# Kernel tuning notes

Hardware: AMD Instinct MI355X
Metric: run time of the kernel (lower is better)

## Reference

```python
import jax, jax.numpy as jnp
import numpy as np

B, T, D = 512, 128, 768
CD, SD, P = 192, 128, 128
FEAT = CD + SD + 1  # 321
LN_EPS = 1e-5


def setup_inputs() -> dict:
    key = jax.random.key(0)
    ks = jax.random.split(key, 10)
    return {
        'H': jax.random.normal(ks[0], (B, T, D), jnp.float32),
        'tt': jax.random.randint(ks[1], (B, T), 0, 2, jnp.int64),
        'attn': jnp.ones((B, T), jnp.int64),
        'Wc': jax.random.normal(ks[2], (CD, 2 * D), jnp.float32) * 0.02,
        'bc': jax.random.normal(ks[3], (CD,), jnp.float32) * 0.02,
        'Ws': jax.random.normal(ks[4], (SD, 2 * D), jnp.float32) * 0.02,
        'bs': jax.random.normal(ks[5], (SD,), jnp.float32) * 0.02,
        'gate': jnp.array([0.5], jnp.float32),
        'ln_g': jnp.ones((FEAT,), jnp.float32),
        'ln_b': jnp.zeros((FEAT,), jnp.float32),
        'Wcls': jax.random.normal(ks[6], (2, FEAT), jnp.float32) * 0.02,
        'bcls': jax.random.normal(ks[7], (2,), jnp.float32) * 0.02,
        'dirs': jax.random.normal(ks[8], (P, D), jnp.float32),
    }


def reference(H, tt, attn, Wc, bc, Ws, bs, gate, ln_g, ln_b, Wcls, bcls, dirs):
    dt = H.dtype
    cls = H[:, 0]                                   # [B, D]
    mask0 = (tt == 0) & (attn == 1)                 # [B, T]
    mask1 = (tt == 1) & (attn == 1)

    def mmean(mask):
        mf = mask.astype(dt)
        s = jnp.einsum('btd,bt->bd', H, mf)
        cnt = jnp.maximum(mask.sum(1, keepdims=True), 1).astype(dt)
        return s / cnt

    rep = jnp.concatenate([cls, mmean(mask0) - mmean(mask1)], axis=1)  # [B, 2D]
    C = rep @ Wc.T + bc
    S = rep @ Ws.T + bs
    g = jax.nn.sigmoid(gate)                        # [1]
    fused = jnp.concatenate([C * (1 - g), S * g], axis=1)  # [B, CD+SD]

    # batched max-sliced W1: project, push masked tokens to +inf, sort along T
    dirs_n = dirs / jnp.linalg.norm(dirs, axis=1, keepdims=True)
    proj = jnp.einsum('btd,pd->btp', H, dirs_n)     # [B, T, P]
    inf = jnp.asarray(jnp.inf, dt)
    xp = jnp.sort(jnp.where(mask0[:, :, None], proj, inf), axis=1)
    yp = jnp.sort(jnp.where(mask1[:, :, None], proj, inf), axis=1)
    n0 = mask0.sum(1)
    n1 = mask1.sum(1)
    mm = jnp.minimum(n0, n1)                        # [B] ragged truncation length
    valid = (jnp.arange(T)[None, :] < mm[:, None])[:, :, None]  # [B, T, 1]
    xs = jnp.where(valid, xp, 0.0)
    ys = jnp.where(valid, yp, 0.0)
    diff = jnp.abs(xs - ys).sum(1) / jnp.maximum(mm, 1)[:, None].astype(dt)  # [B, P]
    d_ot = diff.max(1, keepdims=True)               # [B, 1]

    feat = jnp.concatenate([fused, d_ot], axis=1)   # [B, 321]
    mu = feat.mean(-1, keepdims=True)
    var = feat.var(-1, keepdims=True)
    normed = (feat - mu) / jnp.sqrt(var + LN_EPS) * ln_g + ln_b
    logits = normed @ Wcls.T + bcls                 # [B, 2]

    ortho = jnp.mean((Wc @ Ws.T) ** 2)
    return logits, ortho
```

## Files before the change

### kernel.cpp

```cpp
#include <hip/hip_runtime.h>
#include <hip/hip_bf16.h>

constexpr int B_ = 512;
constexpr int T_ = 128;
constexpr int D_ = 768;
constexpr int CD_ = 192;
constexpr int SD_ = 128;
constexpr int P_ = 128;
constexpr int FEAT_ = 321;
constexpr float LN_EPS_ = 1e-5f;

constexpr size_t REP_SZ   = (size_t)B_ * 2 * D_;
constexpr size_t DN16_FLT = (size_t)P_ * D_ / 2;

typedef __attribute__((ext_vector_type(8))) short short8;
typedef __attribute__((ext_vector_type(4))) float f32x4;

__device__ __forceinline__ unsigned short f2bf(float x) {
    unsigned u = __float_as_uint(x);
    return (unsigned short)((u + 0x7FFFu + ((u >> 16) & 1u)) >> 16);
}
__device__ __forceinline__ float bf2f(unsigned short h) {
    return __uint_as_float((unsigned)h << 16);
}

__global__ __launch_bounds__(256) void k_dirs(const float* __restrict__ dirs,
                                              unsigned short* __restrict__ dn16) {
    int p = blockIdx.x;
    int tid = threadIdx.x;
    float s = 0.f;
    for (int d = tid; d < D_; d += 256) {
        float v = dirs[(size_t)p * D_ + d];
        s = fmaf(v, v, s);
    }
    __shared__ float red[256];
    red[tid] = s;
    __syncthreads();
    for (int off = 128; off > 0; off >>= 1) {
        if (tid < off) red[tid] += red[tid + off];
        __syncthreads();
    }
    float inv = 1.0f / sqrtf(red[0]);
    for (int d = tid; d < D_; d += 256) {
        dn16[(size_t)p * D_ + d] = f2bf(dirs[(size_t)p * D_ + d] * inv);
    }
}

constexpr int NIT_ = 24;
constexpr int BUF_U16_ = 8192;
constexpr int HT_STR_ = 136;

__global__ __launch_bounds__(512, 2) void k_projsort(const float* __restrict__ H,
                                                     const int* __restrict__ tt,
                                                     const int* __restrict__ attn,
                                                     const unsigned short* __restrict__ dn16,
                                                     float* __restrict__ rep,
                                                     float* __restrict__ d_ot) {
    const int b = blockIdx.x;
    const int tid = threadIdx.x;

    __shared__ __align__(16) unsigned short stage[2 * BUF_U16_];
    __shared__ __align__(16) unsigned short Ht[32 * HT_STR_];
    __shared__ __align__(16) unsigned short proj16[T_ * 128];
    __shared__ __align__(16) unsigned short mask16[2 * T_];
    __shared__ float m0s[T_], m1s[T_];
    __shared__ unsigned char pos_s[T_];
    __shared__ int ncnt[2];
    __shared__ float dred[512];

    unsigned char* xb = (unsigned char*)stage;
    unsigned char* yb = xb + 64 * 128;

    const float* Hb = H + (size_t)b * T_ * D_;
    const int srow = tid >> 2;
    const int scp  = tid & 3;
    const int sclog = scp ^ ((srow >> 1) & 3);
    const float* gA = Hb + (size_t)srow * D_ + sclog * 8;
    const unsigned short* gB = dn16 + (size_t)srow * D_ + sclog * 8;
    const int dOff = srow * 32 + scp * 8;

    float4 a0A = *reinterpret_cast<const float4*>(gA);
    float4 a1A = *reinterpret_cast<const float4*>(gA + 4);
    short8 bvA = *reinterpret_cast<const short8*>(gB);
    float4 a0B = *reinterpret_cast<const float4*>(gA + 32);
    float4 a1B = *reinterpret_cast<const float4*>(gA + 36);
    short8 bvB = *reinterpret_cast<const short8*>(gB + 32);

    if (tid < 2) ncnt[tid] = 0;
    __syncthreads();
    if (tid < T_) {
        int t = tt[b * T_ + tid];
        int a = attn[b * T_ + tid];
        float m0 = (t == 0 && a == 1) ? 1.f : 0.f;
        float m1 = (t == 1 && a == 1) ? 1.f : 0.f;
        m0s[tid] = m0;
        m1s[tid] = m1;
        mask16[tid] = (m0 > 0.f) ? 0x3F80u : 0u;
        mask16[T_ + tid] = (m1 > 0.f) ? 0x3F80u : 0u;
        if (m0 > 0.f) atomicAdd(&ncnt[0], 1);
        if (m1 > 0.f) atomicAdd(&ncnt[1], 1);
    }
    __syncthreads();
    const int n0 = ncnt[0], n1 = ncnt[1];
    const int ntot = n0 + n1;
    const float inv0 = 1.f / (float)max(n0, 1);
    const float inv1 = 1.f / (float)max(n1, 1);
    if (tid < T_) {
        float me0 = m0s[tid], me1 = m1s[tid];
        unsigned char pp = 0xFF;
        if (me0 > 0.f || me1 > 0.f) {
            bool g1 = (me1 > 0.f);
            const float* ms = g1 ? m1s : m0s;
            int pos = g1 ? n0 : 0;
            for (int j = 0; j < tid; ++j) pos += (ms[j] > 0.f) ? 1 : 0;
            pp = (unsigned char)pos;
        }
        pos_s[tid] = pp;
    }
    __syncthreads();

    const int wv = tid >> 6;
    const int wr = wv >> 2;
    const int wc = wv & 3;
    const int lane = tid & 63;
    const int fr = lane & 15;
    const int kg = lane >> 4;
    const int fk = kg * 8;
    const int ck = (kg ^ ((fr >> 1) & 3)) * 8;
    const int baseA = (64 * wr + fr) * 32 + ck;
    const int baseB = 4096 + (32 * wc + 16 * 0 + fr) * 32 + ck;
    const bool repw = (wv >= 6);
    const int jf = wv & 1;
    float* repb = rep + (size_t)b * 2 * D_;

    f32x4 acc[4][2];
#pragma unroll
    for (int m = 0; m < 4; ++m)
#pragma unroll
        for (int n = 0; n < 2; ++n) acc[m][n] = (f32x4){0.f, 0.f, 0.f, 0.f};

    auto body = [&](int it, unsigned short* sb, float4& pa0, float4& pa1, short8& pbv) {
        short8 w;
        w[0] = (short)f2bf(pa0.x); w[1] = (short)f2bf(pa0.y);
        w[2] = (short)f2bf(pa0.z); w[3] = (short)f2bf(pa0.w);
        w[4] = (short)f2bf(pa1.x); w[5] = (short)f2bf(pa1.y);
        w[6] = (short)f2bf(pa1.z); w[7] = (short)f2bf(pa1.w);
        *reinterpret_cast<short8*>(sb + dOff) = w;
        *reinterpret_cast<short8*>(sb + 4096 + dOff) = pbv;
#pragma unroll
        for (int j = 0; j < 8; ++j)
            Ht[(sclog * 8 + j) * HT_STR_ + srow] = (unsigned short)w[j];
        if (srow == 0) {
            *reinterpret_cast<float4*>(repb + it * 32 + sclog * 8) = pa0;
            *reinterpret_cast<float4*>(repb + it * 32 + sclog * 8 + 4) = pa1;
        }
        if (it + 2 < NIT_) {
            pa0 = *reinterpret_cast<const float4*>(gA + (it + 2) * 32);
            pa1 = *reinterpret_cast<const float4*>(gA + (it + 2) * 32 + 4);
            pbv = *reinterpret_cast<const short8*>(gB + (it + 2) * 32);
        }
        asm volatile("s_waitcnt lgkmcnt(0)" ::: "memory");
        __builtin_amdgcn_s_barrier();
        asm volatile("" ::: "memory");

        short8 af[4], bf_[2];
#pragma unroll
        for (int m = 0; m < 4; ++m)
            af[m] = *reinterpret_cast<const short8*>(sb + baseA + 512 * m);
#pragma unroll
        for (int n = 0; n < 2; ++n)
            bf_[n] = *reinterpret_cast<const short8*>(sb + baseB + 512 * n);
#pragma unroll
        for (int m = 0; m < 4; ++m)
#pragma unroll
            for (int n = 0; n < 2; ++n)
                acc[m][n] = __builtin_amdgcn_mfma_f32_16x16x32_bf16(af[m], bf_[n], acc[m][n], 0, 0, 0);

        if (repw) {
            f32x4 ar = (f32x4){0.f, 0.f, 0.f, 0.f};
#pragma unroll
            for (int tc = 0; tc < 4; ++tc) {
                short8 am = {0, 0, 0, 0, 0, 0, 0, 0};
                if (fr < 2) am = *reinterpret_cast<const short8*>(&mask16[fr * T_ + tc * 32 + fk]);
                short8 bm = *reinterpret_cast<const short8*>(&Ht[(16 * jf + fr) * HT_STR_ + tc * 32 + fk]);
                ar = __builtin_amdgcn_mfma_f32_16x16x32_bf16(am, bm, ar, 0, 0, 0);
            }
            if (lane < 16) repb[D_ + it * 32 + jf * 16 + lane] = ar[0] * inv0 - ar[1] * inv1;
        }
        asm volatile("" ::: "memory");
        __builtin_amdgcn_s_barrier();
        asm volatile("" ::: "memory");
    };

    for (int i2 = 0; i2 < NIT_ / 2; ++i2) {
        body(2 * i2,     stage,            a0A, a1A, bvA);
        body(2 * i2 + 1, stage + BUF_U16_, a0B, a1B, bvB);
    }

#pragma unroll
    for (int m = 0; m < 4; ++m) {
        int row0 = 64 * wr + 16 * m + kg * 4;
#pragma unroll
        for (int r = 0; r < 4; ++r) {
            int pp = pos_s[row0 + r];
            if (pp != 0xFF) {
#pragma unroll
                for (int n = 0; n < 2; ++n) {
                    int col = 32 * wc + 16 * n + fr;
                    unsigned bb = f2bf(acc[m][n][r]);
                    unsigned su = bb ^ ((bb >> 15) ? 0xFFFFu : 0x8000u);
                    proj16[pp * 128 + col] = (unsigned short)su;
                }
            }
        }
    }
    __syncthreads();

    const int mmv = min(n0, n1);
    const int c = tid & 127;
    const int q = tid >> 7;
#pragma unroll
    for (int pass = 0; pass < 2; ++pass) {
        const int pbase = q * 32 + pass * 16;
        unsigned kv[16];
        int cnt[16];
#pragma unroll
        for (int ii = 0; ii < 16; ++ii) {
            int p = pbase + ii;
            unsigned key = 0xFFFFFFFFu;
            if (p < ntot) {
                unsigned su = proj16[p * 128 + c];
                key = ((unsigned)(p >= n0) << 31) | (su << 8) | (unsigned)p;
            }
            kv[ii] = key;
            cnt[ii] = 0;
        }
        int lo, hi;
        if (pbase + 16 <= n0) { lo = 0;  hi = n0;   }
        else if (pbase >= n0) { lo = n0; hi = ntot; }
        else                  { lo = 0;  hi = ntot; }
        for (int j = lo; j < hi; ++j) {
            unsigned su = proj16[j * 128 + c];
            unsigned kw = ((unsigned)(j >= n0) << 31) | (su << 8) | (unsigned)j;
#pragma unroll
            for (int ii = 0; ii < 16; ++ii) cnt[ii] += (kw < kv[ii]) ? 1 : 0;
        }
#pragma unroll
        for (int ii = 0; ii < 16; ++ii) {
            int p = pbase + ii;
            if (p < ntot) {
                int rank = cnt[ii] - ((p >= n0 && lo == 0) ? n0 : 0);
                if (rank < mmv) {
                    unsigned char* buf = (p >= n0) ? yb : xb;
                    buf[rank * 128 + c] = (unsigned char)p;
                }
            }
        }
    }
    __syncthreads();

    float part = 0.f;
    for (int r = q; r < mmv; r += 4) {
        unsigned sx = proj16[(int)xb[r * 128 + c] * 128 + c];
        unsigned sy = proj16[(int)yb[r * 128 + c] * 128 + c];
        unsigned bx = sx ^ ((sx >> 15) ? 0x8000u : 0xFFFFu);
        unsigned by = sy ^ ((sy >> 15) ? 0x8000u : 0xFFFFu);
        part += fabsf(bf2f((unsigned short)bx) - bf2f((unsigned short)by));
    }
    dred[tid] = part;
    __syncthreads();
    if (tid < 128) {
        float invm = 1.f / (float)max(mmv, 1);
        dred[tid] = (dred[tid] + dred[tid + 128] + dred[tid + 256] + dred[tid + 384]) * invm;
    }
    __syncthreads();
    if (tid < 64) {
        float m = fmaxf(dred[tid], dred[tid + 64]);
#pragma unroll
        for (int off = 32; off > 0; off >>= 1) m = fmaxf(m, __shfl_xor(m, off));
        if (tid == 0) d_ot[b] = m;
    }
}

__global__ __launch_bounds__(320) void k_head(const float* __restrict__ rep,
                                              const float* __restrict__ Wc,
                                              const float* __restrict__ bc,
                                              const float* __restrict__ Ws,
                                              const float* __restrict__ bs,
                                              const float* __restrict__ gate,
                                              const float* __restrict__ lng,
                                              const float* __restrict__ lnb,
                                              const float* __restrict__ Wcls,
                                              const float* __restrict__ bcls,
                                              const float* __restrict__ d_ot,
                                              float* __restrict__ out) {
    int b0 = blockIdx.x * 4;
    int tid = threadIdx.x;
    __shared__ __align__(16) float repS[4 * 1536];
    __shared__ float featS[4 * FEAT_];

    const float4* repg = reinterpret_cast<const float4*>(rep + (size_t)b0 * 1536);
    float4* repl = reinterpret_cast<float4*>(repS);
    for (int i = tid; i < 1536; i += 320) repl[i] = repg[i];
    __syncthreads();

    float g = 1.f / (1.f + expf(-gate[0]));

    {
        int o = tid;
        bool isC = o < CD_;
        const float* w = isC ? (Wc + (size_t)o * 1536) : (Ws + (size_t)(o - CD_) * 1536);
        float bias = isC ? bc[o] : bs[o - CD_];
        float scale = isC ? (1.f - g) : g;
        const float4* w4 = reinterpret_cast<const float4*>(w);
        float a0 = 0.f, a1 = 0.f, a2 = 0.f, a3 = 0.f;
        for (int k4 = 0; k4 < 384; ++k4) {
            float4 wv = w4[k4];
            float4 r0 = repl[k4];
            float4 r1 = repl[384 + k4];
            float4 r2 = repl[768 + k4];
            float4 r3 = repl[1152 + k4];
            a0 += fmaf(wv.x, r0.x, fmaf(wv.y, r0.y, fmaf(wv.z, r0.z, wv.w * r0.w)));
            a1 += fmaf(wv.x, r1.x, fmaf(wv.y, r1.y, fmaf(wv.z, r1.z, wv.w * r1.w)));
            a2 += fmaf(wv.x, r2.x, fmaf(wv.y, r2.y, fmaf(wv.z, r2.z, wv.w * r2.w)));
            a3 += fmaf(wv.x, r3.x, fmaf(wv.y, r3.y, fmaf(wv.z, r3.z, wv.w * r3.w)));
        }
        featS[0 * FEAT_ + o] = (a0 + bias) * scale;
        featS[1 * FEAT_ + o] = (a1 + bias) * scale;
        featS[2 * FEAT_ + o] = (a2 + bias) * scale;
        featS[3 * FEAT_ + o] = (a3 + bias) * scale;
    }
    if (tid < 4) featS[tid * FEAT_ + 320] = d_ot[b0 + tid];
    __syncthreads();

    int w = tid >> 6, lane = tid & 63;
    if (w < 4) {
        const float* f = featS + w * FEAT_;
        float s = 0.f, s2 = 0.f;
        for (int i = lane; i < FEAT_; i += 64) {
            float v = f[i];
            s += v;
            s2 = fmaf(v, v, s2);
        }
#pragma unroll
        for (int off = 32; off > 0; off >>= 1) {
            s += __shfl_xor(s, off);
            s2 += __shfl_xor(s2, off);
        }
        float mu = s * (1.f / (float)FEAT_);
        float var = fmaxf(s2 * (1.f / (float)FEAT_) - mu * mu, 0.f);
        float rstd = 1.0f / sqrtf(var + LN_EPS_);
        float l0 = 0.f, l1 = 0.f;
        for (int i = lane; i < FEAT_; i += 64) {
            float nv = (f[i] - mu) * rstd * lng[i] + lnb[i];
            l0 = fmaf(nv, Wcls[i], l0);
            l1 = fmaf(nv, Wcls[FEAT_ + i], l1);
        }
#pragma unroll
        for (int off = 32; off > 0; off >>= 1) {
            l0 += __shfl_xor(l0, off);
            l1 += __shfl_xor(l1, off);
        }
        if (lane == 0) {
            out[(size_t)(b0 + w) * 2 + 0] = l0 + bcls[0];
            out[(size_t)(b0 + w) * 2 + 1] = l1 + bcls[1];
        }
    }
}

__global__ __launch_bounds__(256) void k_ortho(const float* __restrict__ Wc,
                                               const float* __restrict__ Ws,
                                               float* __restrict__ part) {
    int i = blockIdx.x;
    int tid = threadIdx.x;
    __shared__ float wrow[1536];
    __shared__ float tmp[256];
    for (int k = tid; k < 1536; k += 256) wrow[k] = Wc[(size_t)i * 1536 + k];
    __syncthreads();
    int j = tid & 127, h = tid >> 7;
    const float* wsr = Ws + (size_t)j * 1536 + h * 768;
    const float* wr = wrow + h * 768;
    float s = 0.f;
    for (int k = 0; k < 768; ++k) s = fmaf(wr[k], wsr[k], s);
    tmp[tid] = s;
    __syncthreads();
    if (tid < 128) {
        float d = tmp[tid] + tmp[tid + 128];
        tmp[tid] = d * d;
    }
    __syncthreads();
    for (int off = 64; off > 0; off >>= 1) {
        if (tid < off) tmp[tid] += tmp[tid + off];
        __syncthreads();
    }
    if (tid == 0) part[i] = tmp[0];
}

__global__ __launch_bounds__(256) void k_ortho2(const float* __restrict__ part,
                                                float* __restrict__ out) {
    int tid = threadIdx.x;
    __shared__ float red[256];
    red[tid] = (tid < CD_) ? part[tid] : 0.f;
    __syncthreads();
    for (int off = 128; off > 0; off >>= 1) {
        if (tid < off) red[tid] += red[tid + off];
        __syncthreads();
    }
    if (tid == 0) out[(size_t)B_ * 2] = red[0] / (float)(CD_ * SD_);
}

extern "C" void kernel_launch(void* const* d_in, const int* in_sizes, int n_in,
                              void* d_out, int out_size, void* d_ws, size_t ws_size,
                              hipStream_t stream) {
    const float* H    = (const float*)d_in[0];
    const int*   tt   = (const int*)d_in[1];
    const int*   attn = (const int*)d_in[2];
    const float* Wc   = (const float*)d_in[3];
    const float* bc   = (const float*)d_in[4];
    const float* Ws   = (const float*)d_in[5];
    const float* bs   = (const float*)d_in[6];
    const float* gate = (const float*)d_in[7];
    const float* lng  = (const float*)d_in[8];
    const float* lnb  = (const float*)d_in[9];
    const float* Wcls = (const float*)d_in[10];
    const float* bcls = (const float*)d_in[11];
    const float* dirs = (const float*)d_in[12];

    float* ws    = (float*)d_ws;
    float* rep   = ws;
    unsigned short* dn16 = (unsigned short*)(ws + REP_SZ);
    float* dot   = ws + REP_SZ + DN16_FLT;
    float* part  = dot + B_;
    float* out   = (float*)d_out;

    k_dirs<<<P_, 256, 0, stream>>>(dirs, dn16);
    k_projsort<<<B_, 512, 0, stream>>>(H, tt, attn, dn16, rep, dot);
    k_head<<<B_ / 4, 320, 0, stream>>>(rep, Wc, bc, Ws, bs, gate, lng, lnb, Wcls, bcls, dot, out);
    k_ortho<<<CD_, 256, 0, stream>>>(Wc, Ws, part);
    k_ortho2<<<1, 256, 0, stream>>>(part, out);
}
```

Before: 191.3 us.

## Split projection-sort across two blocks per batch over direction halves

The fused projection and sort kernel now launches two 256-thread blocks per batch row, each handling 64 of the 128 projection directions. Partial max distances go to a two-entry buffer that the head kernel reduces. Mask counts and positions now come from wavefront ballots and popcounts instead of a serial prefix loop. The separate transposed H buffer is dropped, with the masked-mean MMA reading the staged tile directly through strided gathers. The aim is more blocks, higher occupancy and less LDS per block, at the cost of each block reloading the full H tile for its batch row.

```diff
diff --git a/kernel.cpp b/kernel.cpp
--- a/kernel.cpp
+++ b/kernel.cpp
@@ -47,90 +47,97 @@
 }
 
 constexpr int NIT_ = 24;
-constexpr int BUF_U16_ = 8192;
-constexpr int HT_STR_ = 136;
-
-__global__ __launch_bounds__(512, 2) void k_projsort(const float* __restrict__ H,
+constexpr int BUFU_ = 6144;
+
+__global__ __launch_bounds__(256, 4) void k_projsort(const float* __restrict__ H,
                                                      const int* __restrict__ tt,
                                                      const int* __restrict__ attn,
                                                      const unsigned short* __restrict__ dn16,
                                                      float* __restrict__ rep,
-                                                     float* __restrict__ d_ot) {
+                                                     float* __restrict__ dot2) {
     const int b = blockIdx.x;
+    const int y = blockIdx.y;
+    const int p0 = y * 64;
     const int tid = threadIdx.x;
-
-    __shared__ __align__(16) unsigned short stage[2 * BUF_U16_];
-    __shared__ __align__(16) unsigned short Ht[32 * HT_STR_];
-    __shared__ __align__(16) unsigned short proj16[T_ * 128];
-    __shared__ __align__(16) unsigned short mask16[2 * T_];
-    __shared__ float m0s[T_], m1s[T_];
-    __shared__ unsigned char pos_s[T_];
-    __shared__ int ncnt[2];
-    __shared__ float dred[512];
-
+    const int lane = tid & 63;
+    const int w = tid >> 6;
+
+    __shared__ __align__(16) unsigned short stage[2 * BUFU_];
+    __shared__ __align__(16) unsigned short proj16[8192];
     unsigned char* xb = (unsigned char*)stage;
-    unsigned char* yb = xb + 64 * 128;
-
-    const float* Hb = H + (size_t)b * T_ * D_;
-    const int srow = tid >> 2;
-    const int scp  = tid & 3;
-    const int sclog = scp ^ ((srow >> 1) & 3);
-    const float* gA = Hb + (size_t)srow * D_ + sclog * 8;
-    const unsigned short* gB = dn16 + (size_t)srow * D_ + sclog * 8;
-    const int dOff = srow * 32 + scp * 8;
-
-    float4 a0A = *reinterpret_cast<const float4*>(gA);
-    float4 a1A = *reinterpret_cast<const float4*>(gA + 4);
-    short8 bvA = *reinterpret_cast<const short8*>(gB);
-    float4 a0B = *reinterpret_cast<const float4*>(gA + 32);
-    float4 a1B = *reinterpret_cast<const float4*>(gA + 36);
-    short8 bvB = *reinterpret_cast<const short8*>(gB + 32);
-
-    if (tid < 2) ncnt[tid] = 0;
-    __syncthreads();
-    if (tid < T_) {
-        int t = tt[b * T_ + tid];
-        int a = attn[b * T_ + tid];
-        float m0 = (t == 0 && a == 1) ? 1.f : 0.f;
-        float m1 = (t == 1 && a == 1) ? 1.f : 0.f;
-        m0s[tid] = m0;
-        m1s[tid] = m1;
-        mask16[tid] = (m0 > 0.f) ? 0x3F80u : 0u;
-        mask16[T_ + tid] = (m1 > 0.f) ? 0x3F80u : 0u;
-        if (m0 > 0.f) atomicAdd(&ncnt[0], 1);
-        if (m1 > 0.f) atomicAdd(&ncnt[1], 1);
-    }
-    __syncthreads();
-    const int n0 = ncnt[0], n1 = ncnt[1];
+    unsigned char* yb = xb + 4096;
+    float* dred = (float*)&stage[4096];
+
+    const int srow = tid >> 1;
+    const int cpair = (tid & 1) * 2;
+    const int swz = (srow >> 1) & 3;
+    const int lo_log = (cpair ^ swz) & 2;
+    const float* gA = H + (size_t)b * T_ * D_ + (size_t)srow * D_ + lo_log * 8;
+    const int brow = tid & 63;
+    const int bphys = tid >> 6;
+    const int bl = bphys ^ ((brow >> 1) & 3);
+    const unsigned short* gB = dn16 + (size_t)(p0 + brow) * D_ + bl * 8;
+    const int aOff = srow * 32;
+    const int physA0 = lo_log ^ swz;
+
+    float4 fa0 = *reinterpret_cast<const float4*>(gA);
+    float4 fa1 = *reinterpret_cast<const float4*>(gA + 4);
+    float4 fa2 = *reinterpret_cast<const float4*>(gA + 8);
+    float4 fa3 = *reinterpret_cast<const float4*>(gA + 12);
+    short8 bv = *reinterpret_cast<const short8*>(gB);
+
+    const int wr = w & 1;
+    const int wc2 = w >> 1;
+    const int myt = 64 * wr + lane;
+    int v_tt = tt[b * T_ + myt];
+    int v_at = attn[b * T_ + myt];
+    bool m0 = (v_tt == 0) && (v_at == 1);
+    bool m1 = (v_tt == 1) && (v_at == 1);
+    unsigned long long bal0 = __ballot(m0);
+    unsigned long long bal1 = __ballot(m1);
+    if (w < 2 && lane == 0) {
+        ((unsigned long long*)stage)[w * 2] = bal0;
+        ((unsigned long long*)stage)[w * 2 + 1] = bal1;
+    }
+    if (tid < 128) {
+        proj16[tid] = m0 ? 0x3F80u : 0u;
+        proj16[128 + tid] = m1 ? 0x3F80u : 0u;
+    }
+    __syncthreads();
+    const unsigned long long lo0 = ((unsigned long long*)stage)[0];
+    const unsigned long long lo1 = ((unsigned long long*)stage)[1];
+    const unsigned long long hi0 = ((unsigned long long*)stage)[2];
+    const unsigned long long hi1 = ((unsigned long long*)stage)[3];
+    const int n0 = __popcll(lo0) + __popcll(hi0);
+    const int n1 = __popcll(lo1) + __popcll(hi1);
     const int ntot = n0 + n1;
     const float inv0 = 1.f / (float)max(n0, 1);
     const float inv1 = 1.f / (float)max(n1, 1);
-    if (tid < T_) {
-        float me0 = m0s[tid], me1 = m1s[tid];
-        unsigned char pp = 0xFF;
-        if (me0 > 0.f || me1 > 0.f) {
-            bool g1 = (me1 > 0.f);
-            const float* ms = g1 ? m1s : m0s;
-            int pos = g1 ? n0 : 0;
-            for (int j = 0; j < tid; ++j) pos += (ms[j] > 0.f) ? 1 : 0;
-            pp = (unsigned char)pos;
-        }
-        pos_s[tid] = pp;
-    }
-    __syncthreads();
-
-    const int wv = tid >> 6;
-    const int wr = wv >> 2;
-    const int wc = wv & 3;
-    const int lane = tid & 63;
+    unsigned long long below = (lane == 63) ? 0xFFFFFFFFFFFFFFFFull >> 1
+                                            : ((1ull << lane) - 1ull);
+    below = (1ull << lane) - 1ull;
+    int mypos = 0xFF;
+    if (m0) mypos = (wr ? __popcll(lo0) : 0) + __popcll((wr ? hi0 : lo0) & below);
+    else if (m1) mypos = n0 + (wr ? __popcll(lo1) : 0) + __popcll((wr ? hi1 : lo1) & below);
+    __syncthreads();
+
     const int fr = lane & 15;
     const int kg = lane >> 4;
-    const int fk = kg * 8;
-    const int ck = (kg ^ ((fr >> 1) & 3)) * 8;
-    const int baseA = (64 * wr + fr) * 32 + ck;
-    const int baseB = 4096 + (32 * wc + 16 * 0 + fr) * 32 + ck;
-    const bool repw = (wv >= 6);
-    const int jf = wv & 1;
+    int addrA[4], addrB[2];
+#pragma unroll
+    for (int m = 0; m < 4; ++m) {
+        int row = 64 * wr + 16 * m + fr;
+        addrA[m] = row * 32 + (kg ^ ((row >> 1) & 3)) * 8;
+    }
+#pragma unroll
+    for (int n = 0; n < 2; ++n) {
+        int row = 32 * wc2 + 16 * n + fr;
+        addrB[n] = 4096 + row * 32 + (kg ^ ((row >> 1) & 3)) * 8;
+    }
+    const bool repy = (y == 0);
+    const int grp = w & 1;
+    const int dl = grp * 16 + fr;
+    const int dch = dl >> 3, dsub = dl & 7;
     float* repb = rep + (size_t)b * 2 * D_;
 
     f32x4 acc[4][2];
@@ -139,25 +146,34 @@
 #pragma unroll
         for (int n = 0; n < 2; ++n) acc[m][n] = (f32x4){0.f, 0.f, 0.f, 0.f};
 
-    auto body = [&](int it, unsigned short* sb, float4& pa0, float4& pa1, short8& pbv) {
-        short8 w;
-        w[0] = (short)f2bf(pa0.x); w[1] = (short)f2bf(pa0.y);
-        w[2] = (short)f2bf(pa0.z); w[3] = (short)f2bf(pa0.w);
-        w[4] = (short)f2bf(pa1.x); w[5] = (short)f2bf(pa1.y);
-        w[6] = (short)f2bf(pa1.z); w[7] = (short)f2bf(pa1.w);
-        *reinterpret_cast<short8*>(sb + dOff) = w;
-        *reinterpret_cast<short8*>(sb + 4096 + dOff) = pbv;
-#pragma unroll
-        for (int j = 0; j < 8; ++j)
-            Ht[(sclog * 8 + j) * HT_STR_ + srow] = (unsigned short)w[j];
-        if (srow == 0) {
-            *reinterpret_cast<float4*>(repb + it * 32 + sclog * 8) = pa0;
-            *reinterpret_cast<float4*>(repb + it * 32 + sclog * 8 + 4) = pa1;
-        }
-        if (it + 2 < NIT_) {
-            pa0 = *reinterpret_cast<const float4*>(gA + (it + 2) * 32);
-            pa1 = *reinterpret_cast<const float4*>(gA + (it + 2) * 32 + 4);
-            pbv = *reinterpret_cast<const short8*>(gB + (it + 2) * 32);
+    for (int it = 0; it < NIT_; ++it) {
+        const int base = (it & 1) * BUFU_;
+        short8 w0, w1;
+        w0[0] = (short)f2bf(fa0.x); w0[1] = (short)f2bf(fa0.y);
+        w0[2] = (short)f2bf(fa0.z); w0[3] = (short)f2bf(fa0.w);
+        w0[4] = (short)f2bf(fa1.x); w0[5] = (short)f2bf(fa1.y);
+        w0[6] = (short)f2bf(fa1.z); w0[7] = (short)f2bf(fa1.w);
+        w1[0] = (short)f2bf(fa2.x); w1[1] = (short)f2bf(fa2.y);
+        w1[2] = (short)f2bf(fa2.z); w1[3] = (short)f2bf(fa2.w);
+        w1[4] = (short)f2bf(fa3.x); w1[5] = (short)f2bf(fa3.y);
+        w1[6] = (short)f2bf(fa3.z); w1[7] = (short)f2bf(fa3.w);
+        *reinterpret_cast<short8*>(&stage[base + aOff + physA0 * 8]) = w0;
+        *reinterpret_cast<short8*>(&stage[base + aOff + (physA0 ^ 1) * 8]) = w1;
+        *reinterpret_cast<short8*>(&stage[base + 4096 + brow * 32 + bphys * 8]) = bv;
+        if (repy && srow == 0) {
+            float* cd = repb + it * 32 + lo_log * 8;
+            *reinterpret_cast<float4*>(cd)     = fa0;
+            *reinterpret_cast<float4*>(cd + 4) = fa1;
+            *reinterpret_cast<float4*>(cd + 8) = fa2;
+            *reinterpret_cast<float4*>(cd + 12) = fa3;
+        }
+        if (it + 1 < NIT_) {
+            int k = (it + 1) * 32;
+            fa0 = *reinterpret_cast<const float4*>(gA + k);
+            fa1 = *reinterpret_cast<const float4*>(gA + k + 4);
+            fa2 = *reinterpret_cast<const float4*>(gA + k + 8);
+            fa3 = *reinterpret_cast<const float4*>(gA + k + 12);
+            bv = *reinterpret_cast<const short8*>(gB + k);
         }
         asm volatile("s_waitcnt lgkmcnt(0)" ::: "memory");
         __builtin_amdgcn_s_barrier();
@@ -166,50 +182,52 @@
         short8 af[4], bf_[2];
 #pragma unroll
         for (int m = 0; m < 4; ++m)
-            af[m] = *reinterpret_cast<const short8*>(sb + baseA + 512 * m);
+            af[m] = *reinterpret_cast<const short8*>(&stage[base + addrA[m]]);
 #pragma unroll
         for (int n = 0; n < 2; ++n)
-            bf_[n] = *reinterpret_cast<const short8*>(sb + baseB + 512 * n);
+            bf_[n] = *reinterpret_cast<const short8*>(&stage[base + addrB[n]]);
 #pragma unroll
         for (int m = 0; m < 4; ++m)
 #pragma unroll
             for (int n = 0; n < 2; ++n)
                 acc[m][n] = __builtin_amdgcn_mfma_f32_16x16x32_bf16(af[m], bf_[n], acc[m][n], 0, 0, 0);
 
-        if (repw) {
+        if (repy && (((it & 1) == 0) == (w < 2))) {
             f32x4 ar = (f32x4){0.f, 0.f, 0.f, 0.f};
 #pragma unroll
             for (int tc = 0; tc < 4; ++tc) {
+                int tbase = tc * 32 + kg * 8;
                 short8 am = {0, 0, 0, 0, 0, 0, 0, 0};
-                if (fr < 2) am = *reinterpret_cast<const short8*>(&mask16[fr * T_ + tc * 32 + fk]);
-                short8 bm = *reinterpret_cast<const short8*>(&Ht[(16 * jf + fr) * HT_STR_ + tc * 32 + fk]);
+                if (fr < 2) am = *reinterpret_cast<const short8*>(&proj16[fr * 128 + tbase]);
+                short8 bm;
+#pragma unroll
+                for (int j = 0; j < 8; ++j) {
+                    int t = tbase + j;
+                    bm[j] = (short)stage[base + t * 32 + (dch ^ ((t >> 1) & 3)) * 8 + dsub];
+                }
                 ar = __builtin_amdgcn_mfma_f32_16x16x32_bf16(am, bm, ar, 0, 0, 0);
             }
-            if (lane < 16) repb[D_ + it * 32 + jf * 16 + lane] = ar[0] * inv0 - ar[1] * inv1;
+            if (lane < 16)
+                repb[D_ + it * 32 + grp * 16 + lane] = ar[0] * inv0 - ar[1] * inv1;
         }
         asm volatile("" ::: "memory");
         __builtin_amdgcn_s_barrier();
         asm volatile("" ::: "memory");
-    };
-
-    for (int i2 = 0; i2 < NIT_ / 2; ++i2) {
-        body(2 * i2,     stage,            a0A, a1A, bvA);
-        body(2 * i2 + 1, stage + BUF_U16_, a0B, a1B, bvB);
     }
 
 #pragma unroll
     for (int m = 0; m < 4; ++m) {
-        int row0 = 64 * wr + 16 * m + kg * 4;
 #pragma unroll
         for (int r = 0; r < 4; ++r) {
-            int pp = pos_s[row0 + r];
+            int rowlane = 16 * m + kg * 4 + r;
+            int pp = __shfl(mypos, rowlane);
             if (pp != 0xFF) {
 #pragma unroll
                 for (int n = 0; n < 2; ++n) {
-                    int col = 32 * wc + 16 * n + fr;
+                    int col = 32 * wc2 + 16 * n + fr;
                     unsigned bb = f2bf(acc[m][n][r]);
                     unsigned su = bb ^ ((bb >> 15) ? 0xFFFFu : 0x8000u);
-                    proj16[pp * 128 + col] = (unsigned short)su;
+                    proj16[pp * 64 + col] = (unsigned short)su;
                 }
             }
         }
@@ -217,8 +235,8 @@
     __syncthreads();
 
     const int mmv = min(n0, n1);
-    const int c = tid & 127;
-    const int q = tid >> 7;
+    const int c = tid & 63;
+    const int q = tid >> 6;
 #pragma unroll
     for (int pass = 0; pass < 2; ++pass) {
         const int pbase = q * 32 + pass * 16;
@@ -229,7 +247,7 @@
             int p = pbase + ii;
             unsigned key = 0xFFFFFFFFu;
             if (p < ntot) {
-                unsigned su = proj16[p * 128 + c];
+                unsigned su = proj16[p * 64 + c];
                 key = ((unsigned)(p >= n0) << 31) | (su << 8) | (unsigned)p;
             }
             kv[ii] = key;
@@ -240,7 +258,7 @@
         else if (pbase >= n0) { lo = n0; hi = ntot; }
         else                  { lo = 0;  hi = ntot; }
         for (int j = lo; j < hi; ++j) {
-            unsigned su = proj16[j * 128 + c];
+            unsigned su = proj16[j * 64 + c];
             unsigned kw = ((unsigned)(j >= n0) << 31) | (su << 8) | (unsigned)j;
 #pragma unroll
             for (int ii = 0; ii < 16; ++ii) cnt[ii] += (kw < kv[ii]) ? 1 : 0;
@@ -252,7 +270,7 @@
                 int rank = cnt[ii] - ((p >= n0 && lo == 0) ? n0 : 0);
                 if (rank < mmv) {
                     unsigned char* buf = (p >= n0) ? yb : xb;
-                    buf[rank * 128 + c] = (unsigned char)p;
+                    buf[rank * 64 + c] = (unsigned char)p;
                 }
             }
         }
@@ -261,24 +279,21 @@
 
     float part = 0.f;
     for (int r = q; r < mmv; r += 4) {
-        unsigned sx = proj16[(int)xb[r * 128 + c] * 128 + c];
-        unsigned sy = proj16[(int)yb[r * 128 + c] * 128 + c];
+        unsigned sx = proj16[(int)xb[r * 64 + c] * 64 + c];
+        unsigned sy = proj16[(int)yb[r * 64 + c] * 64 + c];
         unsigned bx = sx ^ ((sx >> 15) ? 0x8000u : 0xFFFFu);
-        unsigned by = sy ^ ((sy >> 15) ? 0x8000u : 0xFFFFu);
-        part += fabsf(bf2f((unsigned short)bx) - bf2f((unsigned short)by));
+        unsigned byv = sy ^ ((sy >> 15) ? 0x8000u : 0xFFFFu);
+        part += fabsf(bf2f((unsigned short)bx) - bf2f((unsigned short)byv));
     }
     dred[tid] = part;
     __syncthreads();
-    if (tid < 128) {
+    if (tid < 64) {
         float invm = 1.f / (float)max(mmv, 1);
-        dred[tid] = (dred[tid] + dred[tid + 128] + dred[tid + 256] + dred[tid + 384]) * invm;
-    }
-    __syncthreads();
-    if (tid < 64) {
-        float m = fmaxf(dred[tid], dred[tid + 64]);
+        float s = (dred[tid] + dred[tid + 64] + dred[tid + 128] + dred[tid + 192]) * invm;
+        float m = s;
 #pragma unroll
         for (int off = 32; off > 0; off >>= 1) m = fmaxf(m, __shfl_xor(m, off));
-        if (tid == 0) d_ot[b] = m;
+        if (tid == 0) dot2[b * 2 + y] = m;
     }
 }
 
@@ -292,7 +307,7 @@
                                               const float* __restrict__ lnb,
                                               const float* __restrict__ Wcls,
                                               const float* __restrict__ bcls,
-                                              const float* __restrict__ d_ot,
+                                              const float* __restrict__ dot2,
                                               float* __restrict__ out) {
     int b0 = blockIdx.x * 4;
     int tid = threadIdx.x;
@@ -330,7 +345,10 @@
         featS[2 * FEAT_ + o] = (a2 + bias) * scale;
         featS[3 * FEAT_ + o] = (a3 + bias) * scale;
     }
-    if (tid < 4) featS[tid * FEAT_ + 320] = d_ot[b0 + tid];
+    if (tid < 4) {
+        int bb = b0 + tid;
+        featS[tid * FEAT_ + 320] = fmaxf(dot2[bb * 2], dot2[bb * 2 + 1]);
+    }
     __syncthreads();
 
     int w = tid >> 6, lane = tid & 63;
@@ -429,13 +447,13 @@
     float* ws    = (float*)d_ws;
     float* rep   = ws;
     unsigned short* dn16 = (unsigned short*)(ws + REP_SZ);
-    float* dot   = ws + REP_SZ + DN16_FLT;
-    float* part  = dot + B_;
+    float* dot2  = ws + REP_SZ + DN16_FLT;
+    float* part  = dot2 + 2 * B_;
     float* out   = (float*)d_out;
 
     k_dirs<<<P_, 256, 0, stream>>>(dirs, dn16);
-    k_projsort<<<B_, 512, 0, stream>>>(H, tt, attn, dn16, rep, dot);
-    k_head<<<B_ / 4, 320, 0, stream>>>(rep, Wc, bc, Ws, bs, gate, lng, lnb, Wcls, bcls, dot, out);
+    k_projsort<<<dim3(B_, 2), 256, 0, stream>>>(H, tt, attn, dn16, rep, dot2);
+    k_head<<<B_ / 4, 320, 0, stream>>>(rep, Wc, bc, Ws, bs, gate, lng, lnb, Wcls, bcls, dot2, out);
     k_ortho<<<CD_, 256, 0, stream>>>(Wc, Ws, part);
     k_ortho2<<<1, 256, 0, stream>>>(part, out);
 }
```

After: 208.2 us. +8.8%, slower.

## Split projection into bf16 prep kernel and direct-to-LDS async MFMA pipeline

Applied to the files above, without the earlier changes.

Adds a k_prep kernel that streams H once, writes the CLS and masked-mean rep rows, and stores a pre-swizzled bf16 copy of H in workspace. k_projsort then reads bf16 H and dirs with global_load_lds into a triple-buffered LDS ring, and computes token positions with wave ballots instead of a serial prefix loop. The goal is to take the fp32-to-bf16 conversion, the transposed Ht staging and the mask MFMA out of the inner loop and to overlap loads with compute. In exchange it adds an extra write and read of a bf16 H copy through global memory, and may need to run in batch chunks sized by the workspace.

```diff
diff --git a/kernel.cpp b/kernel.cpp
--- a/kernel.cpp
+++ b/kernel.cpp
@@ -12,6 +12,8 @@
 
 constexpr size_t REP_SZ   = (size_t)B_ * 2 * D_;
 constexpr size_t DN16_FLT = (size_t)P_ * D_ / 2;
+constexpr size_t FIXED_FLT = REP_SZ + DN16_FLT + B_ + CD_;
+constexpr size_t H16_PER_B = (size_t)T_ * D_ * 2;
 
 typedef __attribute__((ext_vector_type(8))) short short8;
 typedef __attribute__((ext_vector_type(4))) float f32x4;
@@ -41,51 +43,22 @@
         __syncthreads();
     }
     float inv = 1.0f / sqrtf(red[0]);
+    const int sz = ((p >> 1) & 3) << 3;
     for (int d = tid; d < D_; d += 256) {
-        dn16[(size_t)p * D_ + d] = f2bf(dirs[(size_t)p * D_ + d] * inv);
-    }
-}
-
-constexpr int NIT_ = 24;
-constexpr int BUF_U16_ = 8192;
-constexpr int HT_STR_ = 136;
-
-__global__ __launch_bounds__(512, 2) void k_projsort(const float* __restrict__ H,
-                                                     const int* __restrict__ tt,
-                                                     const int* __restrict__ attn,
-                                                     const unsigned short* __restrict__ dn16,
-                                                     float* __restrict__ rep,
-                                                     float* __restrict__ d_ot) {
-    const int b = blockIdx.x;
+        dn16[(size_t)p * D_ + (d ^ sz)] = f2bf(dirs[(size_t)p * D_ + d] * inv);
+    }
+}
+
+__global__ __launch_bounds__(192) void k_prep(const float* __restrict__ H,
+                                              const int* __restrict__ tt,
+                                              const int* __restrict__ attn,
+                                              float* __restrict__ rep,
+                                              unsigned short* __restrict__ h16,
+                                              int bOff) {
+    const int b = bOff + blockIdx.x;
     const int tid = threadIdx.x;
-
-    __shared__ __align__(16) unsigned short stage[2 * BUF_U16_];
-    __shared__ __align__(16) unsigned short Ht[32 * HT_STR_];
-    __shared__ __align__(16) unsigned short proj16[T_ * 128];
-    __shared__ __align__(16) unsigned short mask16[2 * T_];
     __shared__ float m0s[T_], m1s[T_];
-    __shared__ unsigned char pos_s[T_];
     __shared__ int ncnt[2];
-    __shared__ float dred[512];
-
-    unsigned char* xb = (unsigned char*)stage;
-    unsigned char* yb = xb + 64 * 128;
-
-    const float* Hb = H + (size_t)b * T_ * D_;
-    const int srow = tid >> 2;
-    const int scp  = tid & 3;
-    const int sclog = scp ^ ((srow >> 1) & 3);
-    const float* gA = Hb + (size_t)srow * D_ + sclog * 8;
-    const unsigned short* gB = dn16 + (size_t)srow * D_ + sclog * 8;
-    const int dOff = srow * 32 + scp * 8;
-
-    float4 a0A = *reinterpret_cast<const float4*>(gA);
-    float4 a1A = *reinterpret_cast<const float4*>(gA + 4);
-    short8 bvA = *reinterpret_cast<const short8*>(gB);
-    float4 a0B = *reinterpret_cast<const float4*>(gA + 32);
-    float4 a1B = *reinterpret_cast<const float4*>(gA + 36);
-    short8 bvB = *reinterpret_cast<const short8*>(gB + 32);
-
     if (tid < 2) ncnt[tid] = 0;
     __syncthreads();
     if (tid < T_) {
@@ -95,43 +68,107 @@
         float m1 = (t == 1 && a == 1) ? 1.f : 0.f;
         m0s[tid] = m0;
         m1s[tid] = m1;
-        mask16[tid] = (m0 > 0.f) ? 0x3F80u : 0u;
-        mask16[T_ + tid] = (m1 > 0.f) ? 0x3F80u : 0u;
         if (m0 > 0.f) atomicAdd(&ncnt[0], 1);
         if (m1 > 0.f) atomicAdd(&ncnt[1], 1);
     }
     __syncthreads();
-    const int n0 = ncnt[0], n1 = ncnt[1];
-    const int ntot = n0 + n1;
-    const float inv0 = 1.f / (float)max(n0, 1);
-    const float inv1 = 1.f / (float)max(n1, 1);
-    if (tid < T_) {
-        float me0 = m0s[tid], me1 = m1s[tid];
-        unsigned char pp = 0xFF;
-        if (me0 > 0.f || me1 > 0.f) {
-            bool g1 = (me1 > 0.f);
-            const float* ms = g1 ? m1s : m0s;
-            int pos = g1 ? n0 : 0;
-            for (int j = 0; j < tid; ++j) pos += (ms[j] > 0.f) ? 1 : 0;
-            pp = (unsigned char)pos;
-        }
-        pos_s[tid] = pp;
-    }
-    __syncthreads();
-
-    const int wv = tid >> 6;
-    const int wr = wv >> 2;
-    const int wc = wv & 3;
+    const float inv0 = 1.f / (float)max(ncnt[0], 1);
+    const float inv1 = 1.f / (float)max(ncnt[1], 1);
+    const float* Hb = H + (size_t)b * T_ * D_;
+    unsigned short* h16b = h16 + (size_t)blockIdx.x * T_ * D_;
+    float* repb = rep + (size_t)b * 2 * D_;
+    const int d0 = tid * 4;
+
+    float4 h = *reinterpret_cast<const float4*>(Hb + d0);
+    *reinterpret_cast<float4*>(repb + d0) = h;
+    float s0x = h.x * m0s[0], s0y = h.y * m0s[0], s0z = h.z * m0s[0], s0w = h.w * m0s[0];
+    float s1x = h.x * m1s[0], s1y = h.y * m1s[0], s1z = h.z * m1s[0], s1w = h.w * m1s[0];
+    {
+        ushort4 v;
+        v.x = f2bf(h.x); v.y = f2bf(h.y); v.z = f2bf(h.z); v.w = f2bf(h.w);
+        *reinterpret_cast<ushort4*>(h16b + d0) = v;
+    }
+#pragma unroll 4
+    for (int t = 1; t < T_; ++t) {
+        h = *reinterpret_cast<const float4*>(Hb + (size_t)t * D_ + d0);
+        float m0 = m0s[t], m1 = m1s[t];
+        s0x = fmaf(h.x, m0, s0x); s1x = fmaf(h.x, m1, s1x);
+        s0y = fmaf(h.y, m0, s0y); s1y = fmaf(h.y, m1, s1y);
+        s0z = fmaf(h.z, m0, s0z); s1z = fmaf(h.z, m1, s1z);
+        s0w = fmaf(h.w, m0, s0w); s1w = fmaf(h.w, m1, s1w);
+        ushort4 v;
+        v.x = f2bf(h.x); v.y = f2bf(h.y); v.z = f2bf(h.z); v.w = f2bf(h.w);
+        int dsw = d0 ^ (((t >> 1) & 3) << 3);
+        *reinterpret_cast<ushort4*>(h16b + (size_t)t * D_ + dsw) = v;
+    }
+    float4 r;
+    r.x = s0x * inv0 - s1x * inv1;
+    r.y = s0y * inv0 - s1y * inv1;
+    r.z = s0z * inv0 - s1z * inv1;
+    r.w = s0w * inv0 - s1w * inv1;
+    *reinterpret_cast<float4*>(repb + D_ + d0) = r;
+}
+
+constexpr int NIT_ = 24;
+
+__global__ __launch_bounds__(512) void k_projsort(const int* __restrict__ tt,
+                                                  const int* __restrict__ attn,
+                                                  const unsigned short* __restrict__ h16,
+                                                  const unsigned short* __restrict__ dn16,
+                                                  float* __restrict__ d_ot,
+                                                  int bOff) {
+    const int b = bOff + blockIdx.x;
+    const int tid = threadIdx.x;
     const int lane = tid & 63;
+    const int w = tid >> 6;
+    const int wr = w >> 2;
+    const int wc = w & 3;
     const int fr = lane & 15;
     const int kg = lane >> 4;
-    const int fk = kg * 8;
-    const int ck = (kg ^ ((fr >> 1) & 3)) * 8;
-    const int baseA = (64 * wr + fr) * 32 + ck;
-    const int baseB = 4096 + (32 * wc + 16 * 0 + fr) * 32 + ck;
-    const bool repw = (wv >= 6);
-    const int jf = wv & 1;
-    float* repb = rep + (size_t)b * 2 * D_;
+
+    __shared__ __align__(16) unsigned short ldsbuf[24576];
+    __shared__ float dred[512];
+    unsigned short* proj16 = ldsbuf;
+    unsigned char* xb = (unsigned char*)(ldsbuf + 16384);
+    unsigned char* yb = xb + 8192;
+
+    const int myt = 64 * wr + lane;
+    int vt = tt[b * T_ + myt];
+    int va = attn[b * T_ + myt];
+    bool m0 = (vt == 0) && (va == 1);
+    bool m1 = (vt == 1) && (va == 1);
+    unsigned long long bal0 = __ballot(m0);
+    unsigned long long bal1 = __ballot(m1);
+    unsigned long long* xch = (unsigned long long*)dred;
+    if (lane == 0 && (w == 0 || w == 4)) {
+        xch[wr * 2] = bal0;
+        xch[wr * 2 + 1] = bal1;
+    }
+    __syncthreads();
+    const unsigned long long lo0 = xch[0], lo1 = xch[1], hi0 = xch[2], hi1 = xch[3];
+    const int n0 = __popcll(lo0) + __popcll(hi0);
+    const int n1 = __popcll(lo1) + __popcll(hi1);
+    const int ntot = n0 + n1;
+    unsigned long long below = (1ull << lane) - 1ull;
+    int mypos = 0xFF;
+    if (m0) mypos = (wr ? __popcll(lo0) : 0) + __popcll((wr ? hi0 : lo0) & below);
+    else if (m1) mypos = n0 + (wr ? __popcll(lo1) : 0) + __popcll((wr ? hi1 : lo1) & below);
+    __syncthreads();
+
+    const unsigned short* gAp = h16 + (size_t)blockIdx.x * T_ * D_ + (size_t)(tid >> 2) * D_ + (tid & 3) * 8;
+    const unsigned short* gBp = dn16 + (size_t)(tid >> 2) * D_ + (tid & 3) * 8;
+
+    int addrA[4], addrB[2];
+#pragma unroll
+    for (int m = 0; m < 4; ++m) {
+        int row = 64 * wr + 16 * m + fr;
+        addrA[m] = row * 32 + (kg ^ ((row >> 1) & 3)) * 8;
+    }
+#pragma unroll
+    for (int n = 0; n < 2; ++n) {
+        int row = 32 * wc + 16 * n + fr;
+        addrB[n] = 4096 + row * 32 + (kg ^ ((row >> 1) & 3)) * 8;
+    }
 
     f32x4 acc[4][2];
 #pragma unroll
@@ -139,70 +176,45 @@
 #pragma unroll
         for (int n = 0; n < 2; ++n) acc[m][n] = (f32x4){0.f, 0.f, 0.f, 0.f};
 
-    auto body = [&](int it, unsigned short* sb, float4& pa0, float4& pa1, short8& pbv) {
-        short8 w;
-        w[0] = (short)f2bf(pa0.x); w[1] = (short)f2bf(pa0.y);
-        w[2] = (short)f2bf(pa0.z); w[3] = (short)f2bf(pa0.w);
-        w[4] = (short)f2bf(pa1.x); w[5] = (short)f2bf(pa1.y);
-        w[6] = (short)f2bf(pa1.z); w[7] = (short)f2bf(pa1.w);
-        *reinterpret_cast<short8*>(sb + dOff) = w;
-        *reinterpret_cast<short8*>(sb + 4096 + dOff) = pbv;
-#pragma unroll
-        for (int j = 0; j < 8; ++j)
-            Ht[(sclog * 8 + j) * HT_STR_ + srow] = (unsigned short)w[j];
-        if (srow == 0) {
-            *reinterpret_cast<float4*>(repb + it * 32 + sclog * 8) = pa0;
-            *reinterpret_cast<float4*>(repb + it * 32 + sclog * 8 + 4) = pa1;
-        }
-        if (it + 2 < NIT_) {
-            pa0 = *reinterpret_cast<const float4*>(gA + (it + 2) * 32);
-            pa1 = *reinterpret_cast<const float4*>(gA + (it + 2) * 32 + 4);
-            pbv = *reinterpret_cast<const short8*>(gB + (it + 2) * 32);
-        }
-        asm volatile("s_waitcnt lgkmcnt(0)" ::: "memory");
+    auto issue = [&](int it2) {
+        const int bufo = (it2 % 3) * 8192;
+        __builtin_amdgcn_global_load_lds((const void*)(gAp + it2 * 32),
+                                         (void*)(&ldsbuf[bufo + w * 512]), 16, 0, 0);
+        __builtin_amdgcn_global_load_lds((const void*)(gBp + it2 * 32),
+                                         (void*)(&ldsbuf[bufo + 4096 + w * 512]), 16, 0, 0);
+    };
+    issue(0);
+    issue(1);
+
+    for (int it = 0; it < NIT_; ++it) {
+        if (it < NIT_ - 1) asm volatile("s_waitcnt vmcnt(2)" ::: "memory");
+        else               asm volatile("s_waitcnt vmcnt(0)" ::: "memory");
         __builtin_amdgcn_s_barrier();
         asm volatile("" ::: "memory");
-
+        if (it + 2 < NIT_) issue(it + 2);
+        const int bufo = (it % 3) * 8192;
         short8 af[4], bf_[2];
 #pragma unroll
         for (int m = 0; m < 4; ++m)
-            af[m] = *reinterpret_cast<const short8*>(sb + baseA + 512 * m);
+            af[m] = *reinterpret_cast<const short8*>(&ldsbuf[bufo + addrA[m]]);
 #pragma unroll
         for (int n = 0; n < 2; ++n)
-            bf_[n] = *reinterpret_cast<const short8*>(sb + baseB + 512 * n);
+            bf_[n] = *reinterpret_cast<const short8*>(&ldsbuf[bufo + addrB[n]]);
 #pragma unroll
         for (int m = 0; m < 4; ++m)
 #pragma unroll
             for (int n = 0; n < 2; ++n)
                 acc[m][n] = __builtin_amdgcn_mfma_f32_16x16x32_bf16(af[m], bf_[n], acc[m][n], 0, 0, 0);
-
-        if (repw) {
-            f32x4 ar = (f32x4){0.f, 0.f, 0.f, 0.f};
-#pragma unroll
-            for (int tc = 0; tc < 4; ++tc) {
-                short8 am = {0, 0, 0, 0, 0, 0, 0, 0};
-                if (fr < 2) am = *reinterpret_cast<const short8*>(&mask16[fr * T_ + tc * 32 + fk]);
-                short8 bm = *reinterpret_cast<const short8*>(&Ht[(16 * jf + fr) * HT_STR_ + tc * 32 + fk]);
-                ar = __builtin_amdgcn_mfma_f32_16x16x32_bf16(am, bm, ar, 0, 0, 0);
-            }
-            if (lane < 16) repb[D_ + it * 32 + jf * 16 + lane] = ar[0] * inv0 - ar[1] * inv1;
-        }
         asm volatile("" ::: "memory");
-        __builtin_amdgcn_s_barrier();
-        asm volatile("" ::: "memory");
-    };
-
-    for (int i2 = 0; i2 < NIT_ / 2; ++i2) {
-        body(2 * i2,     stage,            a0A, a1A, bvA);
-        body(2 * i2 + 1, stage + BUF_U16_, a0B, a1B, bvB);
-    }
+    }
+    __syncthreads();
 
 #pragma unroll
     for (int m = 0; m < 4; ++m) {
-        int row0 = 64 * wr + 16 * m + kg * 4;
 #pragma unroll
         for (int r = 0; r < 4; ++r) {
-            int pp = pos_s[row0 + r];
+            int rowlane = 16 * m + kg * 4 + r;
+            int pp = __shfl(mypos, rowlane);
             if (pp != 0xFF) {
 #pragma unroll
                 for (int n = 0; n < 2; ++n) {
@@ -264,8 +276,8 @@
         unsigned sx = proj16[(int)xb[r * 128 + c] * 128 + c];
         unsigned sy = proj16[(int)yb[r * 128 + c] * 128 + c];
         unsigned bx = sx ^ ((sx >> 15) ? 0x8000u : 0xFFFFu);
-        unsigned by = sy ^ ((sy >> 15) ? 0x8000u : 0xFFFFu);
-        part += fabsf(bf2f((unsigned short)bx) - bf2f((unsigned short)by));
+        unsigned byv = sy ^ ((sy >> 15) ? 0x8000u : 0xFFFFu);
+        part += fabsf(bf2f((unsigned short)bx) - bf2f((unsigned short)byv));
     }
     dred[tid] = part;
     __syncthreads();
@@ -431,10 +443,21 @@
     unsigned short* dn16 = (unsigned short*)(ws + REP_SZ);
     float* dot   = ws + REP_SZ + DN16_FLT;
     float* part  = dot + B_;
+    unsigned short* h16 = (unsigned short*)(ws + FIXED_FLT);
     float* out   = (float*)d_out;
 
+    size_t availB = (ws_size > FIXED_FLT * 4) ? (ws_size - FIXED_FLT * 4) : 0;
+    int maxB = (int)(availB / H16_PER_B);
+    int chunk = B_;
+    while (chunk > maxB && chunk > 1) chunk >>= 1;
+    if (chunk > maxB) chunk = 1;
+
     k_dirs<<<P_, 256, 0, stream>>>(dirs, dn16);
-    k_projsort<<<B_, 512, 0, stream>>>(H, tt, attn, dn16, rep, dot);
+    for (int c = 0; c < B_; c += chunk) {
+        int nb = min(chunk, B_ - c);
+        k_prep<<<nb, 192, 0, stream>>>(H, tt, attn, rep, h16, c);
+        k_projsort<<<nb, 512, 0, stream>>>(tt, attn, h16, dn16, dot, c);
+    }
     k_head<<<B_ / 4, 320, 0, stream>>>(rep, Wc, bc, Ws, bs, gate, lng, lnb, Wcls, bcls, dot, out);
     k_ortho<<<CD_, 256, 0, stream>>>(Wc, Ws, part);
     k_ortho2<<<1, 256, 0, stream>>>(part, out);
```

Measured after the change: 267.7 us. 1.4x slower.
